# Optimization experiments

Measured on AMD Instinct MI355X. Metric: run time of the kernel, lower is better.

The kernel has to match this reference:

```python
import jax, jax.numpy as jnp
import numpy as np

N_EMBD = 384
NUM_HEADS = 6
HEAD_SIZE = 64


def setup_inputs() -> dict:
    key = jax.random.key(0)
    k1, k2, k3, k4 = jax.random.split(key, 4)
    B, T = 32, 1024
    x = jax.random.normal(k1, (B, T, N_EMBD), dtype=jnp.float32)
    # torch Linear(n_embd, 3*n_embd, bias=False): store as [in, out]
    s_attn = 1.0 / np.sqrt(N_EMBD)
    W_attn = jax.random.uniform(k2, (N_EMBD, 3 * N_EMBD), dtype=jnp.float32, minval=-s_attn, maxval=s_attn)
    W_proj = jax.random.uniform(k3, (N_EMBD, N_EMBD), dtype=jnp.float32, minval=-s_attn, maxval=s_attn)
    b_proj = jax.random.uniform(k4, (N_EMBD,), dtype=jnp.float32, minval=-s_attn, maxval=s_attn)
    return {"x": x, "W_attn": W_attn, "W_proj": W_proj, "b_proj": b_proj}


def reference(x, W_attn, W_proj, b_proj):
    B, T, C = x.shape
    H, D = NUM_HEADS, HEAD_SIZE
    qkv = x @ W_attn                      # [B, T, 3C]
    q, k, v = jnp.split(qkv, 3, axis=2)   # each [B, T, C]
    # [B, H, T, D]
    q = q.reshape(B, T, H, D).transpose(0, 2, 1, 3)
    k = k.reshape(B, T, H, D).transpose(0, 2, 1, 3)
    v = v.reshape(B, T, H, D).transpose(0, 2, 1, 3)
    scale = 1.0 / jnp.sqrt(jnp.asarray(D, dtype=x.dtype))
    scores = jnp.einsum("bhqd,bhkd->bhqk", q, k) * scale  # [B, H, T, T]
    causal = jnp.tril(jnp.ones((T, T), dtype=bool))
    scores = jnp.where(causal, scores, jnp.asarray(-jnp.inf, dtype=scores.dtype))
    attn = jax.nn.softmax(scores, axis=-1)
    y = jnp.einsum("bhqk,bhkd->bhqd", attn, v)             # [B, H, T, D]
    y = y.transpose(0, 2, 1, 3).reshape(B, T, C)
    # dropout is inactive in eval mode
    return y @ W_proj + b_proj
```

## Files before the change

### kernel.cpp

```cpp
#include <hip/hip_runtime.h>
#include <hip/hip_bf16.h>

#define DEV __device__ __forceinline__

typedef __attribute__((ext_vector_type(4))) float f32x4;
typedef __bf16 bf16x8 __attribute__((ext_vector_type(8)));

static DEV unsigned short f2bf(float f) {
    union { float f; unsigned u; } x; x.f = f;
    unsigned r = x.u + 0x7fffu + ((x.u >> 16) & 1u);
    return (unsigned short)(r >> 16);
}

static DEV f32x4 zero4() { f32x4 v; v[0] = 0.f; v[1] = 0.f; v[2] = 0.f; v[3] = 0.f; return v; }

#define GL1(p) ((const __attribute__((address_space(1))) void*)(p))
#define LDS3(p) ((__attribute__((address_space(3))) void*)(p))


__global__ __launch_bounds__(256) void k_prep(
    const float* __restrict__ x, unsigned short* __restrict__ xb,
    const float* __restrict__ Wa, unsigned short* __restrict__ WaT,
    const float* __restrict__ Wp, unsigned short* __restrict__ WpT)
{
    int i = blockIdx.x * 256 + threadIdx.x;
    if (i < 3145728) {
        float4 v = reinterpret_cast<const float4*>(x)[i];
        ushort4 o;
        o.x = f2bf(v.x); o.y = f2bf(v.y); o.z = f2bf(v.z); o.w = f2bf(v.w);
        reinterpret_cast<ushort4*>(xb)[i] = o;
    } else if (i < 3145728 + 442368) {
        int j = i - 3145728;
        int n = j / 384, k = j - n * 384;
        WaT[j] = f2bf(Wa[(size_t)k * 1152 + n]);
    } else if (i < 3145728 + 442368 + 147456) {
        int j = i - (3145728 + 442368);
        int n = j / 384, k = j - n * 384;
        WpT[j] = f2bf(Wp[(size_t)k * 384 + n]);
    }
}


template <int EPI>
__global__ __launch_bounds__(256) void k_gemm(
    const unsigned short* __restrict__ A,
    const unsigned short* __restrict__ B,
    unsigned short* __restrict__ Qb, unsigned short* __restrict__ Kb, unsigned short* __restrict__ Vtb,
    const float* __restrict__ bias, float* __restrict__ Out)
{
    const int K = 384;
    __shared__ unsigned short lA[128][64];
    __shared__ unsigned short lB[128][64];

    int tid = threadIdx.x;
    int m0 = blockIdx.x * 128;
    int n0 = blockIdx.y * 128;
    int w = tid >> 6, lane = tid & 63;
    int wm = (w >> 1) * 64, wn = (w & 1) * 64;
    int lr = lane & 15, lg = lane >> 4;

    f32x4 acc[4][4];
#pragma unroll
    for (int i = 0; i < 4; i++)
#pragma unroll
        for (int j = 0; j < 4; j++) acc[i][j] = zero4();

    const int lrow = lane >> 3;
    const int lcol = (lane & 7) * 8;

    for (int kb = 0; kb < K; kb += 64) {
        __syncthreads();
#pragma unroll
        for (int c = 0; c < 4; ++c) {
            int rb = (w * 4 + c) * 8;
            __builtin_amdgcn_global_load_lds(GL1(&A[(size_t)(m0 + rb + lrow) * K + kb + lcol]),
                                             LDS3(&lA[rb][0]), 16, 0, 0);
            __builtin_amdgcn_global_load_lds(GL1(&B[(size_t)(n0 + rb + lrow) * K + kb + lcol]),
                                             LDS3(&lB[rb][0]), 16, 0, 0);
        }
        __syncthreads();

        bf16x8 af[4][2], bfr[4][2];
#pragma unroll
        for (int kc = 0; kc < 2; ++kc) {
#pragma unroll
            for (int t = 0; t < 4; ++t) {
                af[t][kc]  = *(const bf16x8*)&lA[wm + t * 16 + lr][kc * 32 + lg * 8];
                bfr[t][kc] = *(const bf16x8*)&lB[wn + t * 16 + lr][kc * 32 + lg * 8];
            }
        }
#pragma unroll
        for (int kc = 0; kc < 2; ++kc)
#pragma unroll
            for (int mt = 0; mt < 4; ++mt)
#pragma unroll
                for (int nt = 0; nt < 4; ++nt)
                    acc[mt][nt] = __builtin_amdgcn_mfma_f32_16x16x32_bf16(af[mt][kc], bfr[nt][kc], acc[mt][nt], 0, 0, 0);
    }

#pragma unroll
    for (int mt = 0; mt < 4; ++mt) {
#pragma unroll
        for (int nt = 0; nt < 4; ++nt) {
#pragma unroll
            for (int r = 0; r < 4; ++r) {
                int row = m0 + wm + mt * 16 + lg * 4 + r;
                int col = n0 + wn + nt * 16 + lr;
                float v = acc[mt][nt][r];
                if (EPI == 0) {
                    int which = col / 384;
                    int c = col - which * 384;
                    int hh = c >> 6, d = c & 63;
                    int bb = row >> 10, t = row & 1023;
                    size_t bh = (size_t)bb * 6 + hh;
                    if (which == 0) {
                        int qt = t >> 5, fmt = (t >> 4) & 1;
                        int kc = (d >> 5) & 1, e = d & 7;
                        int ln = (t & 15) + 16 * ((d >> 3) & 3);
                        Qb[((((bh * 32 + qt) * 2 + fmt) * 2 + kc) * 64 + ln) * 8 + e] = f2bf(v * 0.18033688f);
                    } else if (which == 1) {
                        int ktt = t >> 6, fnt = (t >> 4) & 3;
                        int kc = (d >> 5) & 1, e = d & 7;
                        int ln = (t & 15) + 16 * ((d >> 3) & 3);
                        Kb[((((bh * 16 + ktt) * 4 + fnt) * 2 + kc) * 64 + ln) * 8 + e] = f2bf(v);
                    } else {
                        int ktt = t >> 6, kc = (t >> 5) & 1, e = t & 7;
                        int fnt = d >> 4;
                        int ln = (d & 15) + 16 * ((t >> 3) & 3);
                        Vtb[((((bh * 16 + ktt) * 4 + fnt) * 2 + kc) * 64 + ln) * 8 + e] = f2bf(v);
                    }
                } else {
                    Out[(size_t)row * 384 + col] = v + bias[col];
                }
            }
        }
    }
}


template <int NTM, bool MASK>
static DEV void attn_tile(
    const unsigned short* lKt, const unsigned short* lVt, unsigned short* lPw,
    const bf16x8 (&qf)[2][2], f32x4 (&o)[2][4], float (&ls)[2],
    int kt, int qw, int lane)
{
    constexpr int KCM = NTM / 2;
    const int lr = lane & 15, lg = lane >> 4;

    bf16x8 kf[NTM][2];
#pragma unroll
    for (int nt = 0; nt < NTM; ++nt)
#pragma unroll
        for (int kc = 0; kc < 2; ++kc)
            kf[nt][kc] = *(const bf16x8*)&lKt[(nt * 2 + kc) * 512 + lane * 8];

    bf16x8 vf[4][KCM];
#pragma unroll
    for (int nt = 0; nt < 4; ++nt)
#pragma unroll
        for (int kc = 0; kc < KCM; ++kc)
            vf[nt][kc] = *(const bf16x8*)&lVt[(nt * 2 + kc) * 512 + lane * 8];

    f32x4 st[2][NTM];
#pragma unroll
    for (int mt = 0; mt < 2; ++mt)
#pragma unroll
        for (int nt = 0; nt < NTM; ++nt) st[mt][nt] = zero4();

#pragma unroll
    for (int kc = 0; kc < 2; ++kc)
#pragma unroll
        for (int mt = 0; mt < 2; ++mt)
#pragma unroll
            for (int nt = 0; nt < NTM; ++nt)
                st[mt][nt] = __builtin_amdgcn_mfma_f32_16x16x32_bf16(kf[nt][kc], qf[mt][kc], st[mt][nt], 0, 0, 0);

#pragma unroll
    for (int mt = 0; mt < 2; ++mt) {
#pragma unroll
        for (int nt = 0; nt < NTM; ++nt) {
            union { __bf16 hh[4]; uint2 u; } pk;
            float e[4];
#pragma unroll
            for (int r = 0; r < 4; ++r) {
                float ev = __builtin_amdgcn_exp2f(st[mt][nt][r]);
                if (MASK) {
                    int kg = kt * 64 + nt * 16 + lg * 4 + r;
                    int qg = qw + mt * 16 + lr;
                    if (kg > qg) ev = 0.f;
                }
                e[r] = ev;
                pk.hh[r] = (__bf16)ev;
            }
            ls[mt] += (e[0] + e[1]) + (e[2] + e[3]);
            int ln2 = lr + 16 * ((nt & 1) * 2 + (lg >> 1));
            *(uint2*)&lPw[(mt * 2 + (nt >> 1)) * 512 + ln2 * 8 + (lg & 1) * 4] = pk.u;
        }
    }

    bf16x8 pf[2][KCM];
#pragma unroll
    for (int mt = 0; mt < 2; ++mt)
#pragma unroll
        for (int kc = 0; kc < KCM; ++kc)
            pf[mt][kc] = *(const bf16x8*)&lPw[(mt * 2 + kc) * 512 + lane * 8];

#pragma unroll
    for (int mt = 0; mt < 2; ++mt)
#pragma unroll
        for (int nt = 0; nt < 4; ++nt)
#pragma unroll
            for (int kc = 0; kc < KCM; ++kc)
                o[mt][nt] = __builtin_amdgcn_mfma_f32_16x16x32_bf16(pf[mt][kc], vf[nt][kc], o[mt][nt], 0, 0, 0);
}

__global__ __launch_bounds__(256, 3) void k_attn(
    const unsigned short* __restrict__ Qf,
    const unsigned short* __restrict__ Kf,
    const unsigned short* __restrict__ Vf,
    unsigned short* __restrict__ Y)
{
    __shared__ unsigned short lK[2][4096];
    __shared__ unsigned short lV[2][4096];
    __shared__ unsigned short lPf[4][2048];

    const int tid = threadIdx.x;
    const int w = tid >> 6, lane = tid & 63;
    const int lr = lane & 15, lg = lane >> 4;
    const int bh = blockIdx.x;
    const int g = 7 - blockIdx.y;
    const int qt = 4 * g + w;
    const int qw = qt * 32;
    const int nkt = qt / 2 + 1;
    const int nsteps = 2 * g + 2;
    const int b = bh / 6, h = bh - b * 6;

    const unsigned short* Kbh = Kf + (size_t)bh * 65536;
    const unsigned short* Vbh = Vf + (size_t)bh * 65536;

    bf16x8 qf[2][2];
#pragma unroll
    for (int mt = 0; mt < 2; ++mt)
#pragma unroll
        for (int kc = 0; kc < 2; ++kc)
            qf[mt][kc] = *(const bf16x8*)&Qf[((((size_t)bh * 32 + qt) * 2 + mt) * 2 + kc) * 512 + lane * 8];

    f32x4 o[2][4];
    float ls[2] = {0.f, 0.f};
#pragma unroll
    for (int mt = 0; mt < 2; ++mt)
#pragma unroll
        for (int nt = 0; nt < 4; ++nt) o[mt][nt] = zero4();

#pragma unroll
    for (int i = 0; i < 2; ++i) {
        __builtin_amdgcn_global_load_lds(GL1(Kbh + (size_t)w * 1024 + i * 512 + lane * 8),
                                         LDS3(&lK[0][w * 1024 + i * 512]), 16, 0, 0);
        __builtin_amdgcn_global_load_lds(GL1(Vbh + (size_t)w * 1024 + i * 512 + lane * 8),
                                         LDS3(&lV[0][w * 1024 + i * 512]), 16, 0, 0);
    }

    for (int kt = 0; kt < nsteps; ++kt) {
        __syncthreads();
        if (kt + 1 < nsteps) {
            int nb = (kt + 1) & 1;
#pragma unroll
            for (int i = 0; i < 2; ++i) {
                __builtin_amdgcn_global_load_lds(GL1(Kbh + (size_t)(kt + 1) * 4096 + w * 1024 + i * 512 + lane * 8),
                                                 LDS3(&lK[nb][w * 1024 + i * 512]), 16, 0, 0);
                __builtin_amdgcn_global_load_lds(GL1(Vbh + (size_t)(kt + 1) * 4096 + w * 1024 + i * 512 + lane * 8),
                                                 LDS3(&lV[nb][w * 1024 + i * 512]), 16, 0, 0);
            }
        }
        if (kt < nkt) {
            const unsigned short* lKt = lK[kt & 1];
            const unsigned short* lVt = lV[kt & 1];
            if (kt == nkt - 1) {
                if (qt & 1) attn_tile<4, true>(lKt, lVt, lPf[w], qf, o, ls, kt, qw, lane);
                else        attn_tile<2, true>(lKt, lVt, lPf[w], qf, o, ls, kt, qw, lane);
            } else {
                attn_tile<4, false>(lKt, lVt, lPf[w], qf, o, ls, kt, qw, lane);
            }
        }
    }

    float inv[2];
#pragma unroll
    for (int mt = 0; mt < 2; ++mt) {
        float s = ls[mt];
        s += __shfl_xor(s, 16);
        s += __shfl_xor(s, 32);
        inv[mt] = 1.0f / s;
    }
#pragma unroll
    for (int mt = 0; mt < 2; ++mt) {
        float iv[4];
#pragma unroll
        for (int r = 0; r < 4; ++r) iv[r] = __shfl(inv[mt], lg * 4 + r);
#pragma unroll
        for (int nt = 0; nt < 4; ++nt)
#pragma unroll
            for (int r = 0; r < 4; ++r) {
                int qrow = qw + mt * 16 + lg * 4 + r;
                int col = h * 64 + nt * 16 + lr;
                Y[((size_t)b * 1024 + qrow) * 384 + col] = f2bf(o[mt][nt][r] * iv[r]);
            }
    }
}


extern "C" void kernel_launch(void* const* d_in, const int* in_sizes, int n_in,
                              void* d_out, int out_size, void* d_ws, size_t ws_size,
                              hipStream_t stream)
{
    const float* x  = (const float*)d_in[0];
    const float* Wa = (const float*)d_in[1];
    const float* Wp = (const float*)d_in[2];
    const float* bp = (const float*)d_in[3];
    float* out = (float*)d_out;

    char* ws = (char*)d_ws;
    unsigned short* xb  = (unsigned short*)(ws);
    unsigned short* WaT = (unsigned short*)(ws + 25165824);
    unsigned short* WpT = (unsigned short*)(ws + 26050560);
    unsigned short* Qb  = (unsigned short*)(ws + 26345472);
    unsigned short* Kb  = (unsigned short*)(ws + 51511296);
    unsigned short* Vtb = (unsigned short*)(ws + 76677120);

    k_prep<<<14592, 256, 0, stream>>>(x, xb, Wa, WaT, Wp, WpT);
    k_gemm<0><<<dim3(256, 9), 256, 0, stream>>>(xb, WaT, Qb, Kb, Vtb, nullptr, nullptr);
    k_attn<<<dim3(192, 8), 256, 0, stream>>>(Qb, Kb, Vtb, xb);
    k_gemm<1><<<dim3(256, 3), 256, 0, stream>>>(xb, WpT, nullptr, nullptr, nullptr, bp, out);
}
```

Baseline: 153.0 us.

## Swizzle GEMM LDS tiles and vectorize epilogue stores via MFMA operand swap

Applies an XOR swizzle to the LDS layout of the GEMM tiles so the fragment reads avoid bank conflicts. The MFMA operands are swapped for the Q/K and projection paths, so each lane holds 4 consecutive output columns and can write packed 8-byte bf16 or 16-byte fp32 stores instead of scalar ones. The V path keeps the original operand order, since its transposed layout already has consecutive t per lane. This adds branchy specialization, and correctness depends on the swizzle matching between the global-to-LDS writes and the reads.

```diff
diff --git a/kernel.cpp b/kernel.cpp
--- a/kernel.cpp
+++ b/kernel.cpp
@@ -41,32 +41,20 @@
 }
 
 
-template <int EPI>
-__global__ __launch_bounds__(256) void k_gemm(
+template <int SWAP>
+static DEV void gemm_mainloop(
     const unsigned short* __restrict__ A,
     const unsigned short* __restrict__ B,
-    unsigned short* __restrict__ Qb, unsigned short* __restrict__ Kb, unsigned short* __restrict__ Vtb,
-    const float* __restrict__ bias, float* __restrict__ Out)
+    int m0, int n0, int tid,
+    f32x4 (&acc)[4][4],
+    unsigned short (&lA)[128][64], unsigned short (&lB)[128][64])
 {
     const int K = 384;
-    __shared__ unsigned short lA[128][64];
-    __shared__ unsigned short lB[128][64];
-
-    int tid = threadIdx.x;
-    int m0 = blockIdx.x * 128;
-    int n0 = blockIdx.y * 128;
-    int w = tid >> 6, lane = tid & 63;
-    int wm = (w >> 1) * 64, wn = (w & 1) * 64;
-    int lr = lane & 15, lg = lane >> 4;
-
-    f32x4 acc[4][4];
-#pragma unroll
-    for (int i = 0; i < 4; i++)
-#pragma unroll
-        for (int j = 0; j < 4; j++) acc[i][j] = zero4();
-
+    const int w = tid >> 6, lane = tid & 63;
+    const int wm = (w >> 1) * 64, wn = (w & 1) * 64;
+    const int lr = lane & 15, lg = lane >> 4;
     const int lrow = lane >> 3;
-    const int lcol = (lane & 7) * 8;
+    const int lcol = ((lane & 7) ^ lrow) * 8;
 
     for (int kb = 0; kb < K; kb += 64) {
         __syncthreads();
@@ -85,8 +73,9 @@
         for (int kc = 0; kc < 2; ++kc) {
 #pragma unroll
             for (int t = 0; t < 4; ++t) {
-                af[t][kc]  = *(const bf16x8*)&lA[wm + t * 16 + lr][kc * 32 + lg * 8];
-                bfr[t][kc] = *(const bf16x8*)&lB[wn + t * 16 + lr][kc * 32 + lg * 8];
+                int ga = ((kc * 4 + lg) ^ (lr & 7)) * 8;
+                af[t][kc]  = *(const bf16x8*)&lA[wm + t * 16 + lr][ga];
+                bfr[t][kc] = *(const bf16x8*)&lB[wn + t * 16 + lr][ga];
             }
         }
 #pragma unroll
@@ -95,44 +84,125 @@
             for (int mt = 0; mt < 4; ++mt)
 #pragma unroll
                 for (int nt = 0; nt < 4; ++nt)
-                    acc[mt][nt] = __builtin_amdgcn_mfma_f32_16x16x32_bf16(af[mt][kc], bfr[nt][kc], acc[mt][nt], 0, 0, 0);
-    }
+                    acc[mt][nt] = SWAP
+                        ? __builtin_amdgcn_mfma_f32_16x16x32_bf16(bfr[nt][kc], af[mt][kc], acc[mt][nt], 0, 0, 0)
+                        : __builtin_amdgcn_mfma_f32_16x16x32_bf16(af[mt][kc], bfr[nt][kc], acc[mt][nt], 0, 0, 0);
+    }
+}
+
+
+__global__ __launch_bounds__(256) void k_gemm_qkv(
+    const unsigned short* __restrict__ A,
+    const unsigned short* __restrict__ B,
+    unsigned short* __restrict__ Qb, unsigned short* __restrict__ Kb,
+    unsigned short* __restrict__ Vb)
+{
+    __shared__ unsigned short lA[128][64];
+    __shared__ unsigned short lB[128][64];
+
+    const int tid = threadIdx.x;
+    const int m0 = blockIdx.x * 128, n0 = blockIdx.y * 128;
+    const int w = tid >> 6, lane = tid & 63;
+    const int wm = (w >> 1) * 64, wn = (w & 1) * 64;
+    const int lr = lane & 15, lg = lane >> 4;
+
+    f32x4 acc[4][4];
+#pragma unroll
+    for (int i = 0; i < 4; i++)
+#pragma unroll
+        for (int j = 0; j < 4; j++) acc[i][j] = zero4();
+
+    if (blockIdx.y < 6) {
+        gemm_mainloop<1>(A, B, m0, n0, tid, acc, lA, lB);
+        const int which = blockIdx.y / 3;
+#pragma unroll
+        for (int mt = 0; mt < 4; ++mt) {
+            int row = m0 + wm + mt * 16 + lr;
+            int bb = row >> 10, tloc = row & 1023;
+#pragma unroll
+            for (int nt = 0; nt < 4; ++nt) {
+                int col = n0 + wn + nt * 16 + lg * 4;
+                int c = col - which * 384;
+                int hh = c >> 6, d0 = c & 63;
+                size_t bh = (size_t)bb * 6 + hh;
+                int kc = (d0 >> 5) & 1;
+                int ln = (tloc & 15) + 16 * ((d0 >> 3) & 3);
+                int e0 = d0 & 7;
+                union { __bf16 h4[4]; uint2 u; } pk;
+                if (which == 0) {
+#pragma unroll
+                    for (int r = 0; r < 4; ++r)
+                        pk.h4[r] = (__bf16)(acc[mt][nt][r] * 0.18033688f);
+                    int qt = tloc >> 5, fmt = (tloc >> 4) & 1;
+                    *(uint2*)&Qb[((((bh * 32 + qt) * 2 + fmt) * 2 + kc) * 64 + ln) * 8 + e0] = pk.u;
+                } else {
+#pragma unroll
+                    for (int r = 0; r < 4; ++r)
+                        pk.h4[r] = (__bf16)acc[mt][nt][r];
+                    int ktt = tloc >> 6, fnt = (tloc >> 4) & 3;
+                    *(uint2*)&Kb[((((bh * 16 + ktt) * 4 + fnt) * 2 + kc) * 64 + ln) * 8 + e0] = pk.u;
+                }
+            }
+        }
+    } else {
+        gemm_mainloop<0>(A, B, m0, n0, tid, acc, lA, lB);
+#pragma unroll
+        for (int nt = 0; nt < 4; ++nt) {
+            int col = n0 + wn + nt * 16 + lr;
+            int c = col - 768;
+            int hh = c >> 6, d = c & 63;
+            int fnt = d >> 4;
+#pragma unroll
+            for (int mt = 0; mt < 4; ++mt) {
+                int row0 = m0 + wm + mt * 16 + lg * 4;
+                int bb = row0 >> 10, t0 = row0 & 1023;
+                size_t bh = (size_t)bb * 6 + hh;
+                int ktt = t0 >> 6, kc = (t0 >> 5) & 1, e0 = t0 & 7;
+                int ln = (d & 15) + 16 * ((t0 >> 3) & 3);
+                union { __bf16 h4[4]; uint2 u; } pk;
+#pragma unroll
+                for (int r = 0; r < 4; ++r)
+                    pk.h4[r] = (__bf16)acc[mt][nt][r];
+                *(uint2*)&Vb[((((bh * 16 + ktt) * 4 + fnt) * 2 + kc) * 64 + ln) * 8 + e0] = pk.u;
+            }
+        }
+    }
+}
+
+
+__global__ __launch_bounds__(256) void k_gemm_proj(
+    const unsigned short* __restrict__ A,
+    const unsigned short* __restrict__ B,
+    const float* __restrict__ bias, float* __restrict__ Out)
+{
+    __shared__ unsigned short lA[128][64];
+    __shared__ unsigned short lB[128][64];
+
+    const int tid = threadIdx.x;
+    const int m0 = blockIdx.x * 128, n0 = blockIdx.y * 128;
+    const int w = tid >> 6, lane = tid & 63;
+    const int wm = (w >> 1) * 64, wn = (w & 1) * 64;
+    const int lr = lane & 15, lg = lane >> 4;
+
+    f32x4 acc[4][4];
+#pragma unroll
+    for (int i = 0; i < 4; i++)
+#pragma unroll
+        for (int j = 0; j < 4; j++) acc[i][j] = zero4();
+
+    gemm_mainloop<1>(A, B, m0, n0, tid, acc, lA, lB);
 
 #pragma unroll
     for (int mt = 0; mt < 4; ++mt) {
+        int row = m0 + wm + mt * 16 + lr;
 #pragma unroll
         for (int nt = 0; nt < 4; ++nt) {
-#pragma unroll
-            for (int r = 0; r < 4; ++r) {
-                int row = m0 + wm + mt * 16 + lg * 4 + r;
-                int col = n0 + wn + nt * 16 + lr;
-                float v = acc[mt][nt][r];
-                if (EPI == 0) {
-                    int which = col / 384;
-                    int c = col - which * 384;
-                    int hh = c >> 6, d = c & 63;
-                    int bb = row >> 10, t = row & 1023;
-                    size_t bh = (size_t)bb * 6 + hh;
-                    if (which == 0) {
-                        int qt = t >> 5, fmt = (t >> 4) & 1;
-                        int kc = (d >> 5) & 1, e = d & 7;
-                        int ln = (t & 15) + 16 * ((d >> 3) & 3);
-                        Qb[((((bh * 32 + qt) * 2 + fmt) * 2 + kc) * 64 + ln) * 8 + e] = f2bf(v * 0.18033688f);
-                    } else if (which == 1) {
-                        int ktt = t >> 6, fnt = (t >> 4) & 3;
-                        int kc = (d >> 5) & 1, e = d & 7;
-                        int ln = (t & 15) + 16 * ((d >> 3) & 3);
-                        Kb[((((bh * 16 + ktt) * 4 + fnt) * 2 + kc) * 64 + ln) * 8 + e] = f2bf(v);
-                    } else {
-                        int ktt = t >> 6, kc = (t >> 5) & 1, e = t & 7;
-                        int fnt = d >> 4;
-                        int ln = (d & 15) + 16 * ((t >> 3) & 3);
-                        Vtb[((((bh * 16 + ktt) * 4 + fnt) * 2 + kc) * 64 + ln) * 8 + e] = f2bf(v);
-                    }
-                } else {
-                    Out[(size_t)row * 384 + col] = v + bias[col];
-                }
-            }
+            int col = n0 + wn + nt * 16 + lg * 4;
+            f32x4 bv = *(const f32x4*)&bias[col];
+            f32x4 ov;
+#pragma unroll
+            for (int r = 0; r < 4; ++r) ov[r] = acc[mt][nt][r] + bv[r];
+            *(f32x4*)&Out[(size_t)row * 384 + col] = ov;
         }
     }
 }
@@ -328,7 +398,7 @@
     unsigned short* Vtb = (unsigned short*)(ws + 76677120);
 
     k_prep<<<14592, 256, 0, stream>>>(x, xb, Wa, WaT, Wp, WpT);
-    k_gemm<0><<<dim3(256, 9), 256, 0, stream>>>(xb, WaT, Qb, Kb, Vtb, nullptr, nullptr);
+    k_gemm_qkv<<<dim3(256, 9), 256, 0, stream>>>(xb, WaT, Qb, Kb, Vtb);
     k_attn<<<dim3(192, 8), 256, 0, stream>>>(Qb, Kb, Vtb, xb);
-    k_gemm<1><<<dim3(256, 3), 256, 0, stream>>>(xb, WpT, nullptr, nullptr, nullptr, bp, out);
-}
+    k_gemm_proj<<<dim3(256, 3), 256, 0, stream>>>(xb, WpT, bp, out);
+}
```

New measurement: 125.1 us. 1.22x faster.
